# Performance work log

Measured on AMD Instinct MI355X. Metric: run time of the kernel, lower is better.

## Reference

```python
import jax, jax.numpy as jnp
import numpy as np

S, B, D, H, E, K = 1024, 4, 1024, 16, 3, 2
DFF = 4 * D
DH = D // H


def _layernorm(x, w, b, eps=1e-5):
    mu = jnp.mean(x, axis=-1, keepdims=True)
    var = jnp.var(x, axis=-1, keepdims=True)
    return (x - mu) * jax.lax.rsqrt(var + eps) * w + b


def _quick_gelu(x):
    return x * jax.nn.sigmoid(1.702 * x)


def setup_inputs() -> dict:
    key = jax.random.key(0)
    ks = jax.random.split(key, 8)
    w = lambda k, shape: jax.random.normal(k, shape, dtype=jnp.float32) * 0.02
    return {
        "x": jax.random.normal(ks[0], (S, B, D), dtype=jnp.float32),
        "ln1_w": jnp.ones((D,), jnp.float32), "ln1_b": jnp.zeros((D,), jnp.float32),
        "ln2_w": jnp.ones((D,), jnp.float32), "ln2_b": jnp.zeros((D,), jnp.float32),
        "in_proj_w": w(ks[1], (3 * D, D)), "in_proj_b": jnp.zeros((3 * D,), jnp.float32),
        "out_proj_w": w(ks[2], (D, D)), "out_proj_b": jnp.zeros((D,), jnp.float32),
        "gate_w": w(ks[3], (E, D)),
        "fc_w": w(ks[4], (E, DFF, D)), "fc_b": jnp.zeros((E, DFF), jnp.float32),
        "proj_w": w(ks[5], (E, D, DFF)), "proj_b": jnp.zeros((E, D), jnp.float32),
    }


def _forward(x, ln1_w, ln1_b, ln2_w, ln2_b, in_proj_w, in_proj_b,
             out_proj_w, out_proj_b, gate_w, fc_w, fc_b, proj_w, proj_b):
    s, b, d = x.shape
    # --- causal self-attention (torch nn.MultiheadAttention, seq-first) ---
    h = _layernorm(x, ln1_w, ln1_b)
    qkv = h @ in_proj_w.T + in_proj_b                      # [S,B,3D]
    q, k, v = jnp.split(qkv, 3, axis=-1)
    to_bhsd = lambda t: t.reshape(s, b, H, DH).transpose(1, 2, 0, 3)  # [B,H,S,Dh]
    q, k, v = to_bhsd(q) * (DH ** -0.5), to_bhsd(k), to_bhsd(v)
    mask = jnp.where(jnp.arange(s)[:, None] >= jnp.arange(s)[None, :], 0.0, -jnp.inf)
    scores = jnp.einsum("bhqd,bhkd->bhqk", q, k) + mask    # [B,H,S,S]
    attn = jax.nn.softmax(scores, axis=-1)
    o = jnp.einsum("bhqk,bhkd->bhqd", attn, v)
    o = o.transpose(2, 0, 1, 3).reshape(s, b, d)
    x = x + (o @ out_proj_w.T + out_proj_b)

    # --- MoE routing ---
    hs = _layernorm(x, ln2_w, ln2_b)
    hs_flat = hs.reshape(-1, d)                            # [T,D], T = S*B
    router_logits = hs_flat @ gate_w.T                     # [T,E]
    rw = jax.nn.softmax(router_logits.astype(jnp.float32), axis=-1)
    top_vals, top_idx = jax.lax.top_k(rw, K)               # [T,K]
    top_vals = top_vals / jnp.sum(top_vals, axis=-1, keepdims=True)

    # dense grouped expert FFN (E=3 small, compute-all + masked combine)
    h1 = _quick_gelu(jnp.einsum("td,efd->etf", hs_flat, fc_w) + fc_b[:, None, :])
    expert_out = jnp.einsum("etf,edf->etd", h1, proj_w) + proj_b[:, None, :]  # [E,T,D]
    comb = jnp.sum(jax.nn.one_hot(top_idx, E, dtype=top_vals.dtype) * top_vals[..., None], axis=1)  # [T,E]
    final_hidden_states = jnp.einsum("te,etd->td", comb, expert_out).reshape(s, b, d)
    del final_hidden_states  # NOTE: source computes this but never uses it in the output

    gate_score = jnp.max(top_vals, axis=-1).reshape(s, b, 1)
    out = x * gate_score
    return out, router_logits


def reference(x, ln1_w, ln1_b, ln2_w, ln2_b, in_proj_w, in_proj_b,
              out_proj_w, out_proj_b, gate_w, fc_w, fc_b, proj_w, proj_b):
    return _forward(x, ln1_w, ln1_b, ln2_w, ln2_b, in_proj_w, in_proj_b,
                    out_proj_w, out_proj_b, gate_w, fc_w, fc_b, proj_w, proj_b)
```

## Files before the change

### kernel.cpp

```cpp
#include <hip/hip_runtime.h>
#include <hip/hip_bf16.h>

#define S_DIM 1024
#define B_DIM 4
#define D_DIM 1024
#define H_DIM 16
#define DH    64
#define T_DIM (S_DIM * B_DIM)
#define QKV_N (3 * D_DIM)

using bf16 = __hip_bfloat16;
typedef __attribute__((ext_vector_type(4))) float fx4;
typedef __attribute__((ext_vector_type(8))) short bx8;

__device__ __forceinline__ unsigned short f2bf(float f) {
  union { float f; unsigned int u; } cv; cv.f = f;
  unsigned int u = cv.u;
  unsigned int r = (u + 0x7FFFu + ((u >> 16) & 1u)) >> 16;
  return (unsigned short)r;
}

__device__ __forceinline__ void g2l16(const void* g, void* l) {
  __builtin_amdgcn_global_load_lds(
      (const __attribute__((address_space(1))) unsigned int*)g,
      (__attribute__((address_space(3))) unsigned int*)l, 16, 0, 0);
}

__global__ __launch_bounds__(256) void cast2_f32_bf16(
    const float* __restrict__ a, bf16* __restrict__ da, int an4,
    const float* __restrict__ b, bf16* __restrict__ db, int bn4) {
  const int i = blockIdx.x * 256 + threadIdx.x;
  const float* src; bf16* dst; int j;
  if (i < an4) { src = a; dst = da; j = i; }
  else if (i < an4 + bn4) { src = b; dst = db; j = i - an4; }
  else return;
  const fx4 v = ((const fx4*)src)[j];
  ushort4 u;
  u.x = f2bf(v[0]); u.y = f2bf(v[1]); u.z = f2bf(v[2]); u.w = f2bf(v[3]);
  ((ushort4*)dst)[j] = u;
}

__global__ __launch_bounds__(256) void ln_bf16_kernel(
    const float* __restrict__ x, const float* __restrict__ w,
    const float* __restrict__ bb, bf16* __restrict__ out) {
  const int t = blockIdx.x, tid = threadIdx.x;
  const fx4 v = ((const fx4*)(x + (size_t)t * D_DIM))[tid];
  float s  = v[0] + v[1] + v[2] + v[3];
  float ss = v[0]*v[0] + v[1]*v[1] + v[2]*v[2] + v[3]*v[3];
#pragma unroll
  for (int off = 32; off >= 1; off >>= 1) {
    s  += __shfl_xor(s, off);
    ss += __shfl_xor(ss, off);
  }
  __shared__ float red[8];
  const int wid = tid >> 6, lane = tid & 63;
  if (lane == 0) { red[wid] = s; red[4 + wid] = ss; }
  __syncthreads();
  s  = red[0] + red[1] + red[2] + red[3];
  ss = red[4] + red[5] + red[6] + red[7];
  const float mu = s * (1.f / D_DIM);
  const float rstd = rsqrtf(ss * (1.f / D_DIM) - mu * mu + 1e-5f);
  const fx4 wv = ((const fx4*)w)[tid];
  const fx4 bv = ((const fx4*)bb)[tid];
  ushort4 u;
  u.x = f2bf((v[0] - mu) * rstd * wv[0] + bv[0]);
  u.y = f2bf((v[1] - mu) * rstd * wv[1] + bv[1]);
  u.z = f2bf((v[2] - mu) * rstd * wv[2] + bv[2]);
  u.w = f2bf((v[3] - mu) * rstd * wv[3] + bv[3]);
  ((ushort4*)(out + (size_t)t * D_DIM))[tid] = u;
}

template <int EPI>
__global__ __launch_bounds__(256, 2) void gemm_bt(
    const bf16* __restrict__ A, const bf16* __restrict__ B,
    const float* __restrict__ bias, const float* __restrict__ resid,
    float* __restrict__ C, ushort* __restrict__ qkvb, int N, int K) {
  __shared__ bf16 sA[2][128 * 32];
  __shared__ bf16 sB[2][128 * 32];
  const int tid  = threadIdx.x;
  const int brow = blockIdx.y * 128;
  const int bcol = blockIdx.x * 128;
  const int wid  = tid >> 6;
  const int lane = tid & 63;
  const int wr   = wid >> 1;
  const int wc   = wid & 1;
  const int fr   = lane & 15;
  const int fk   = lane >> 4;

  fx4 acc[4][4];
#pragma unroll
  for (int i = 0; i < 4; ++i)
#pragma unroll
    for (int j = 0; j < 4; ++j) acc[i][j] = 0.f;

  const int arow = tid >> 2;
  const int acol = (tid & 3) * 8;

  auto stage = [&](int buf, int kt) {
#pragma unroll
    for (int is = 0; is < 2; ++is) {
      const int row = is * 64 + arow;
      const int off = row * 64 + acol * 2;
      g2l16(A + (size_t)(brow + row) * K + kt + acol, (char*)sA[buf] + off);
      g2l16(B + (size_t)(bcol + row) * K + kt + acol, (char*)sB[buf] + off);
    }
  };

  stage(0, 0);
  asm volatile("s_waitcnt vmcnt(0)" ::: "memory");
  __builtin_amdgcn_s_barrier();
  asm volatile("" ::: "memory");

  const int nk = K >> 5;
  int cur = 0;
#pragma unroll 1
  for (int ki = 0; ki < nk; ++ki) {
    if (ki + 1 < nk) stage(cur ^ 1, (ki + 1) * 32);
    asm volatile("" ::: "memory");

    bx8 af[4], bfr[4];
#pragma unroll
    for (int mm = 0; mm < 4; ++mm)
      af[mm] = *(const bx8*)(sA[cur] + (wr * 64 + mm * 16 + fr) * 32 + fk * 8);
#pragma unroll
    for (int nn = 0; nn < 4; ++nn)
      bfr[nn] = *(const bx8*)(sB[cur] + (wc * 64 + nn * 16 + fr) * 32 + fk * 8);
#pragma unroll
    for (int mm = 0; mm < 4; ++mm)
#pragma unroll
      for (int nn = 0; nn < 4; ++nn)
        acc[mm][nn] = __builtin_amdgcn_mfma_f32_16x16x32_bf16(
            af[mm], bfr[nn], acc[mm][nn], 0, 0, 0);

    if (ki + 1 < nk) {
      asm volatile("s_waitcnt vmcnt(0)" ::: "memory");
      __builtin_amdgcn_s_barrier();
      asm volatile("" ::: "memory");
    }
    cur ^= 1;
  }

  const int row0 = brow + wr * 64 + fk * 4;
  const int col0 = bcol + wc * 64 + fr;
#pragma unroll
  for (int mm = 0; mm < 4; ++mm) {
#pragma unroll
    for (int nn = 0; nn < 4; ++nn) {
      const int col = col0 + nn * 16;
      const float bv = bias[col];
      if (EPI == 1) {
#pragma unroll
        for (int rr = 0; rr < 4; ++rr) {
          const int row = row0 + mm * 16 + rr;
          C[(size_t)row * N + col] = acc[mm][nn][rr] + bv + resid[(size_t)row * N + col];
        }
      } else {
        const int which = col >> 10;
        const int rem   = col & 1023;
        const int hh    = rem >> 6;
        const int dh    = rem & 63;
        const float scale = (which == 0) ? 0.18033688f : 1.0f;
#pragma unroll
        for (int rr = 0; rr < 4; ++rr) {
          const int row = row0 + mm * 16 + rr;
          const int ss2 = row >> 2, bb2 = row & 3;
          const float v = (acc[mm][nn][rr] + bv) * scale;
          qkvb[(size_t)which * 4194304 +
               ((size_t)(bb2 * 16 + hh)) * 65536 + (size_t)ss2 * 64 + dh] = f2bf(v);
        }
      }
    }
  }
}

__global__ __launch_bounds__(256) void transpose_v(
    const ushort* __restrict__ v, ushort* __restrict__ vt) {
  __shared__ ushort tile[64][65];
  const int g  = blockIdx.x;
  const int bh = g >> 4, st = g & 15;
  const int s0 = st * 64;
  const int tid = threadIdx.x;
  const int r  = tid >> 2;
  const int c0 = (tid & 3) * 16;
  const ushort* src = v + (size_t)bh * 65536 + (size_t)(s0 + r) * 64 + c0;
#pragma unroll
  for (int i = 0; i < 2; ++i) {
    const bx8 d = *(const bx8*)(src + i * 8);
#pragma unroll
    for (int j = 0; j < 8; ++j) tile[r][c0 + i * 8 + j] = (ushort)d[j];
  }
  __syncthreads();
  ushort* dst = vt + (size_t)bh * 65536 + (size_t)r * 1024 + s0 + c0;
  bx8 w0, w1;
#pragma unroll
  for (int j = 0; j < 8; ++j) {
    w0[j] = (short)tile[c0 + j][r];
    w1[j] = (short)tile[c0 + 8 + j][r];
  }
  *(bx8*)dst = w0;
  *(bx8*)(dst + 8) = w1;
}

__global__ __launch_bounds__(256, 4) void attn_mfma(
    const ushort* __restrict__ qb, const ushort* __restrict__ kb,
    const ushort* __restrict__ vtb, ushort* __restrict__ ob) {
  __shared__ __align__(16) char sK[2][8192];
  __shared__ __align__(16) char sVT[2][8192];
  __shared__ __align__(16) char sP[8192];
  const int tid  = threadIdx.x;
  const int wid  = tid >> 6;
  const int lane = tid & 63;
  const int g    = blockIdx.x;
  const int qt   = 15 - (g >> 6);
  const int bh   = g & 63;
  const int b    = bh >> 4, h = bh & 15;
  const int fr   = lane & 15;
  const int fk   = lane >> 4;
  const size_t bhoff = (size_t)bh * 65536;
  char* const sPw = sP + wid * 2048;
  const int swp = (fr & 7) << 4;

  auto stage = [&](int buf, int k0) {
#pragma unroll
    for (int is = 0; is < 2; ++is) {
      const int L    = is * 4096 + tid * 16;
      const int row  = L >> 7;
      const int colb = (L & 127) ^ ((row & 7) << 4);
      g2l16(kb  + bhoff + (size_t)(k0 + row) * 64 + (colb >> 1), sK[buf]  + L);
      g2l16(vtb + bhoff + (size_t)row * 1024 + k0 + (colb >> 1), sVT[buf] + L);
    }
  };

  const int q0w = qt * 64 + wid * 16;
  const ushort* qp = qb + bhoff + (size_t)(q0w + fr) * 64;
  const bx8 qf0 = *(const bx8*)(qp + fk * 8);
  const bx8 qf1 = *(const bx8*)(qp + 32 + fk * 8);
  asm volatile("s_waitcnt vmcnt(0)" ::: "memory");

  fx4 o4[4];
  float m = -3e38f, l = 0.f;
#pragma unroll
  for (int dt = 0; dt < 4; ++dt) o4[dt] = 0.f;

  stage(0, 0);
  int cur = 0;

#pragma unroll 1
  for (int kbk = 0; kbk <= qt; ++kbk) {
    if (kbk < qt) {
      stage(cur ^ 1, (kbk + 1) * 64);
      asm volatile("s_waitcnt vmcnt(4)" ::: "memory");
    } else {
      asm volatile("s_waitcnt vmcnt(0)" ::: "memory");
    }
    __builtin_amdgcn_s_barrier();
    asm volatile("" ::: "memory");
    const char* sKc  = sK[cur];
    const char* sVTc = sVT[cur];

    fx4 s4[4];
    __builtin_amdgcn_s_setprio(1);
#pragma unroll
    for (int kt = 0; kt < 4; ++kt) {
      const int krow = kt * 16 + fr;
      const int sw   = (krow & 7) << 4;
      const bx8 kf0 = *(const bx8*)(sKc + krow * 128 + ((fk * 16) ^ sw));
      const bx8 kf1 = *(const bx8*)(sKc + krow * 128 + ((64 + fk * 16) ^ sw));
      fx4 z = {0.f, 0.f, 0.f, 0.f};
      z = __builtin_amdgcn_mfma_f32_16x16x32_bf16(kf0, qf0, z, 0, 0, 0);
      s4[kt] = __builtin_amdgcn_mfma_f32_16x16x32_bf16(kf1, qf1, z, 0, 0, 0);
    }
    __builtin_amdgcn_s_setprio(0);

    if (kbk == qt) {
      const int qloc = wid * 16 + fr;
#pragma unroll
      for (int kt = 0; kt < 4; ++kt) {
        const int keyb = kt * 16 + fk * 4;
#pragma unroll
        for (int rr = 0; rr < 4; ++rr)
          if (keyb + rr > qloc) s4[kt][rr] = -3e38f;
      }
    }

    float pm = s4[0][0];
#pragma unroll
    for (int kt = 0; kt < 4; ++kt)
#pragma unroll
      for (int rr = 0; rr < 4; ++rr) pm = fmaxf(pm, s4[kt][rr]);
    pm = fmaxf(pm, __shfl_xor(pm, 16));
    pm = fmaxf(pm, __shfl_xor(pm, 32));

    if (__any(pm > m + 11.5f)) {
      const float mn = fmaxf(m, pm);
      const float f  = exp2f(m - mn);
      m = mn;
      l *= f;
      float fq[4];
#pragma unroll
      for (int rr = 0; rr < 4; ++rr) fq[rr] = __shfl(f, fk * 4 + rr);
#pragma unroll
      for (int dt = 0; dt < 4; ++dt)
#pragma unroll
        for (int rr = 0; rr < 4; ++rr) o4[dt][rr] *= fq[rr];
    }

#pragma unroll
    for (int kt = 0; kt < 4; ++kt) {
      union { float f; unsigned u; } a0, a1, a2, a3;
      a0.f = exp2f(s4[kt][0] - m);
      a1.f = exp2f(s4[kt][1] - m);
      a2.f = exp2f(s4[kt][2] - m);
      a3.f = exp2f(s4[kt][3] - m);
      l += (a0.f + a1.f) + (a2.f + a3.f);
      uint2 pk;
      pk.x = (a0.u >> 16) | (a1.u & 0xFFFF0000u);
      pk.y = (a2.u >> 16) | (a3.u & 0xFFFF0000u);
      *(uint2*)(sPw + ((fr * 128 + kt * 32 + fk * 8) ^ swp)) = pk;
    }

    __builtin_amdgcn_s_setprio(1);
#pragma unroll
    for (int c = 0; c < 2; ++c) {
      const bx8 pa = *(const bx8*)(sPw + ((fr * 128 + c * 64 + fk * 16) ^ swp));
#pragma unroll
      for (int dt = 0; dt < 4; ++dt) {
        const int vrow = dt * 16 + fr;
        const bx8 vf = *(const bx8*)(sVTc + vrow * 128 +
                                     ((c * 64 + fk * 16) ^ ((vrow & 7) << 4)));
        o4[dt] = __builtin_amdgcn_mfma_f32_16x16x32_bf16(pa, vf, o4[dt], 0, 0, 0);
      }
    }
    __builtin_amdgcn_s_setprio(0);

    asm volatile("" ::: "memory");
    __builtin_amdgcn_s_barrier();
    asm volatile("" ::: "memory");
    cur ^= 1;
  }

  l += __shfl_xor(l, 16);
  l += __shfl_xor(l, 32);
  const float linv = 1.f / l;
  float lq[4];
#pragma unroll
  for (int rr = 0; rr < 4; ++rr) lq[rr] = __shfl(linv, fk * 4 + rr);

#pragma unroll
  for (int dt = 0; dt < 4; ++dt) {
#pragma unroll
    for (int rr = 0; rr < 4; ++rr) {
      const int qq = q0w + fk * 4 + rr;
      ob[((size_t)qq * 4 + b) * 1024 + h * 64 + dt * 16 + fr] =
          f2bf(o4[dt][rr] * lq[rr]);
    }
  }
}

__global__ __launch_bounds__(256) void final_kernel(
    const float* __restrict__ xn, const float* __restrict__ w,
    const float* __restrict__ bb, const float* __restrict__ gw,
    float* __restrict__ out, float* __restrict__ rlog) {
  const int t = blockIdx.x, tid = threadIdx.x;
  const fx4 v = ((const fx4*)(xn + (size_t)t * D_DIM))[tid];
  float s  = v[0] + v[1] + v[2] + v[3];
  float ss = v[0]*v[0] + v[1]*v[1] + v[2]*v[2] + v[3]*v[3];
#pragma unroll
  for (int off = 32; off >= 1; off >>= 1) {
    s  += __shfl_xor(s, off);
    ss += __shfl_xor(ss, off);
  }
  __shared__ float red[8];
  __shared__ float red2[12];
  const int wid = tid >> 6, lane = tid & 63;
  if (lane == 0) { red[wid] = s; red[4 + wid] = ss; }
  __syncthreads();
  s  = red[0] + red[1] + red[2] + red[3];
  ss = red[4] + red[5] + red[6] + red[7];
  const float mu = s * (1.f / D_DIM);
  const float rstd = rsqrtf(ss * (1.f / D_DIM) - mu * mu + 1e-5f);
  const fx4 wv = ((const fx4*)w)[tid];
  const fx4 bv = ((const fx4*)bb)[tid];
  fx4 hv;
#pragma unroll
  for (int cc = 0; cc < 4; ++cc) hv[cc] = (v[cc] - mu) * rstd * wv[cc] + bv[cc];

  const fx4 w0 = ((const fx4*)(gw           ))[tid];
  const fx4 w1 = ((const fx4*)(gw +     D_DIM))[tid];
  const fx4 w2 = ((const fx4*)(gw + 2 * D_DIM))[tid];
  float g0 = hv[0]*w0[0] + hv[1]*w0[1] + hv[2]*w0[2] + hv[3]*w0[3];
  float g1 = hv[0]*w1[0] + hv[1]*w1[1] + hv[2]*w1[2] + hv[3]*w1[3];
  float g2 = hv[0]*w2[0] + hv[1]*w2[1] + hv[2]*w2[2] + hv[3]*w2[3];
#pragma unroll
  for (int off = 32; off >= 1; off >>= 1) {
    g0 += __shfl_xor(g0, off);
    g1 += __shfl_xor(g1, off);
    g2 += __shfl_xor(g2, off);
  }
  if (lane == 0) { red2[wid] = g0; red2[4 + wid] = g1; red2[8 + wid] = g2; }
  __syncthreads();
  g0 = red2[0] + red2[1] + red2[2]  + red2[3];
  g1 = red2[4] + red2[5] + red2[6]  + red2[7];
  g2 = red2[8] + red2[9] + red2[10] + red2[11];

  const float lmax = fmaxf(g0, fmaxf(g1, g2));
  const float lmin = fminf(g0, fminf(g1, g2));
  const float lmid = (g0 + g1 + g2) - lmax - lmin;
  const float gate = 1.f / (1.f + __expf(lmid - lmax));

  ((fx4*)(out + (size_t)t * D_DIM))[tid] = v * gate;
  if (tid == 0) {
    rlog[(size_t)t * 3 + 0] = g0;
    rlog[(size_t)t * 3 + 1] = g1;
    rlog[(size_t)t * 3 + 2] = g2;
  }
}

extern "C" void kernel_launch(void* const* d_in, const int* in_sizes, int n_in,
                              void* d_out, int out_size, void* d_ws, size_t ws_size,
                              hipStream_t stream) {
  (void)in_sizes; (void)n_in; (void)out_size; (void)ws_size;
  const float* x    = (const float*)d_in[0];
  const float* ln1w = (const float*)d_in[1];
  const float* ln1b = (const float*)d_in[2];
  const float* ln2w = (const float*)d_in[3];
  const float* ln2b = (const float*)d_in[4];
  const float* win  = (const float*)d_in[5];
  const float* bin  = (const float*)d_in[6];
  const float* wout = (const float*)d_in[7];
  const float* bout = (const float*)d_in[8];
  const float* gw   = (const float*)d_in[9];

  char* ws = (char*)d_ws;
  bf16*   w_in_b  = (bf16*)(ws);
  bf16*   w_out_b = (bf16*)(ws + 6291456);
  bf16*   h_b     = (bf16*)(ws + 8388608);
  ushort* o_b     = (ushort*)h_b;
  ushort* qkvb    = (ushort*)(ws + 16777216);
  ushort* q_b     = qkvb;
  ushort* k_b     = qkvb + 4194304;
  ushort* v_b     = qkvb + 8388608;
  float*  xnew    = (float*)(ws + 41943040);
  ushort* vt_b    = (ushort*)(ws + 58720256);

  float* out  = (float*)d_out;
  float* rlog = out + (size_t)T_DIM * D_DIM;

  cast2_f32_bf16<<<4096, 256, 0, stream>>>(win, w_in_b, 786432,
                                           wout, w_out_b, 262144);
  ln_bf16_kernel<<<T_DIM, 256, 0, stream>>>(x, ln1w, ln1b, h_b);
  gemm_bt<2><<<dim3(QKV_N / 128, T_DIM / 128), 256, 0, stream>>>(
      h_b, w_in_b, bin, nullptr, nullptr, qkvb, QKV_N, D_DIM);
  transpose_v<<<1024, 256, 0, stream>>>(v_b, vt_b);
  attn_mfma<<<1024, 256, 0, stream>>>(q_b, k_b, vt_b, o_b);
  gemm_bt<1><<<dim3(D_DIM / 128, T_DIM / 128), 256, 0, stream>>>(
      (const bf16*)o_b, w_out_b, bout, x, xnew, nullptr, D_DIM, D_DIM);
  final_kernel<<<T_DIM, 256, 0, stream>>>(xnew, ln2w, ln2b, gw, out, rlog);
}
```

Before: 115.8 us.

## Pair causal query tiles per attention block, merge prep kernels, narrow out-proj tiles

Attention now runs 512-thread blocks where two groups of four waves handle complementary query tiles (pr and 15-pr), so every block does the same total causal work. Shared K/V staging is reused across both tiles, and blocks are ordered so each XCD keeps to a fixed set of heads. The weight cast and LN1 are merged into one launch, and the output projection gets its own kernel with 128x64 tiles for more blocks. The cost is more idle waves for the short-tile group, which still waits on barriers while the long tile runs, and lower per-block occupancy at 512 threads.

Measured after the change: 115.5 us. Within noise of the previous version (-0.3%).

```diff
diff --git a/kernel.cpp b/kernel.cpp
--- a/kernel.cpp
+++ b/kernel.cpp
@@ -26,24 +26,24 @@
       (__attribute__((address_space(3))) unsigned int*)l, 16, 0, 0);
 }
 
-__global__ __launch_bounds__(256) void cast2_f32_bf16(
-    const float* __restrict__ a, bf16* __restrict__ da, int an4,
-    const float* __restrict__ b, bf16* __restrict__ db, int bn4) {
-  const int i = blockIdx.x * 256 + threadIdx.x;
-  const float* src; bf16* dst; int j;
-  if (i < an4) { src = a; dst = da; j = i; }
-  else if (i < an4 + bn4) { src = b; dst = db; j = i - an4; }
-  else return;
-  const fx4 v = ((const fx4*)src)[j];
-  ushort4 u;
-  u.x = f2bf(v[0]); u.y = f2bf(v[1]); u.z = f2bf(v[2]); u.w = f2bf(v[3]);
-  ((ushort4*)dst)[j] = u;
-}
-
-__global__ __launch_bounds__(256) void ln_bf16_kernel(
+__global__ __launch_bounds__(256) void prep_kernel(
     const float* __restrict__ x, const float* __restrict__ w,
-    const float* __restrict__ bb, bf16* __restrict__ out) {
-  const int t = blockIdx.x, tid = threadIdx.x;
+    const float* __restrict__ bb, bf16* __restrict__ out,
+    const float* __restrict__ win, bf16* __restrict__ winb,
+    const float* __restrict__ wout, bf16* __restrict__ woutb) {
+  const int blk = blockIdx.x, tid = threadIdx.x;
+  if (blk >= 4096) {
+    const int i = (blk - 4096) * 256 + tid;
+    const float* src; bf16* dst; int j;
+    if (i < 786432) { src = win; dst = winb; j = i; }
+    else { src = wout; dst = woutb; j = i - 786432; }
+    const fx4 v = ((const fx4*)src)[j];
+    ushort4 u;
+    u.x = f2bf(v[0]); u.y = f2bf(v[1]); u.z = f2bf(v[2]); u.w = f2bf(v[3]);
+    ((ushort4*)dst)[j] = u;
+    return;
+  }
+  const int t = blk;
   const fx4 v = ((const fx4*)(x + (size_t)t * D_DIM))[tid];
   float s  = v[0] + v[1] + v[2] + v[3];
   float ss = v[0]*v[0] + v[1]*v[1] + v[2]*v[2] + v[3]*v[3];
@@ -70,11 +70,9 @@
   ((ushort4*)(out + (size_t)t * D_DIM))[tid] = u;
 }
 
-template <int EPI>
-__global__ __launch_bounds__(256, 2) void gemm_bt(
+__global__ __launch_bounds__(256, 2) void gemm_qkv(
     const bf16* __restrict__ A, const bf16* __restrict__ B,
-    const float* __restrict__ bias, const float* __restrict__ resid,
-    float* __restrict__ C, ushort* __restrict__ qkvb, int N, int K) {
+    const float* __restrict__ bias, ushort* __restrict__ qkvb, int K) {
   __shared__ bf16 sA[2][128 * 32];
   __shared__ bf16 sB[2][128 * 32];
   const int tid  = threadIdx.x;
@@ -148,26 +146,18 @@
     for (int nn = 0; nn < 4; ++nn) {
       const int col = col0 + nn * 16;
       const float bv = bias[col];
-      if (EPI == 1) {
-#pragma unroll
-        for (int rr = 0; rr < 4; ++rr) {
-          const int row = row0 + mm * 16 + rr;
-          C[(size_t)row * N + col] = acc[mm][nn][rr] + bv + resid[(size_t)row * N + col];
-        }
-      } else {
-        const int which = col >> 10;
-        const int rem   = col & 1023;
-        const int hh    = rem >> 6;
-        const int dh    = rem & 63;
-        const float scale = (which == 0) ? 0.18033688f : 1.0f;
-#pragma unroll
-        for (int rr = 0; rr < 4; ++rr) {
-          const int row = row0 + mm * 16 + rr;
-          const int ss2 = row >> 2, bb2 = row & 3;
-          const float v = (acc[mm][nn][rr] + bv) * scale;
-          qkvb[(size_t)which * 4194304 +
-               ((size_t)(bb2 * 16 + hh)) * 65536 + (size_t)ss2 * 64 + dh] = f2bf(v);
-        }
+      const int which = col >> 10;
+      const int rem   = col & 1023;
+      const int hh    = rem >> 6;
+      const int dh    = rem & 63;
+      const float scale = (which == 0) ? 0.18033688f : 1.0f;
+#pragma unroll
+      for (int rr = 0; rr < 4; ++rr) {
+        const int row = row0 + mm * 16 + rr;
+        const int ss2 = row >> 2, bb2 = row & 3;
+        const float v = (acc[mm][nn][rr] + bv) * scale;
+        qkvb[(size_t)which * 4194304 +
+             ((size_t)(bb2 * 16 + hh)) * 65536 + (size_t)ss2 * 64 + dh] = f2bf(v);
       }
     }
   }
@@ -201,37 +191,39 @@
   *(bx8*)(dst + 8) = w1;
 }
 
-__global__ __launch_bounds__(256, 4) void attn_mfma(
+__global__ __launch_bounds__(512, 4) void attn_mfma(
     const ushort* __restrict__ qb, const ushort* __restrict__ kb,
     const ushort* __restrict__ vtb, ushort* __restrict__ ob) {
   __shared__ __align__(16) char sK[2][8192];
   __shared__ __align__(16) char sVT[2][8192];
-  __shared__ __align__(16) char sP[8192];
+  __shared__ __align__(16) char sP[16384];
   const int tid  = threadIdx.x;
   const int wid  = tid >> 6;
   const int lane = tid & 63;
-  const int g    = blockIdx.x;
-  const int qt   = 15 - (g >> 6);
-  const int bh   = g & 63;
+  const int bid  = blockIdx.x;
+  const int xcd  = bid & 7;
+  const int r2   = bid >> 3;
+  const int pr   = r2 & 7;
+  const int bh   = (r2 >> 3) * 8 + xcd;
   const int b    = bh >> 4, h = bh & 15;
   const int fr   = lane & 15;
   const int fk   = lane >> 4;
   const size_t bhoff = (size_t)bh * 65536;
   char* const sPw = sP + wid * 2048;
   const int swp = (fr & 7) << 4;
+  const int qt_max  = 15 - pr;
+  const int qt_mine = (wid < 4) ? pr : qt_max;
+  const int wid4 = wid & 3;
 
   auto stage = [&](int buf, int k0) {
-#pragma unroll
-    for (int is = 0; is < 2; ++is) {
-      const int L    = is * 4096 + tid * 16;
-      const int row  = L >> 7;
-      const int colb = (L & 127) ^ ((row & 7) << 4);
-      g2l16(kb  + bhoff + (size_t)(k0 + row) * 64 + (colb >> 1), sK[buf]  + L);
-      g2l16(vtb + bhoff + (size_t)row * 1024 + k0 + (colb >> 1), sVT[buf] + L);
-    }
+    const int L    = tid * 16;
+    const int row  = L >> 7;
+    const int colb = (L & 127) ^ ((row & 7) << 4);
+    g2l16(kb  + bhoff + (size_t)(k0 + row) * 64 + (colb >> 1), sK[buf]  + L);
+    g2l16(vtb + bhoff + (size_t)row * 1024 + k0 + (colb >> 1), sVT[buf] + L);
   };
 
-  const int q0w = qt * 64 + wid * 16;
+  const int q0w = qt_mine * 64 + wid4 * 16;
   const ushort* qp = qb + bhoff + (size_t)(q0w + fr) * 64;
   const bx8 qf0 = *(const bx8*)(qp + fk * 8);
   const bx8 qf1 = *(const bx8*)(qp + 32 + fk * 8);
@@ -243,100 +235,102 @@
   for (int dt = 0; dt < 4; ++dt) o4[dt] = 0.f;
 
   stage(0, 0);
-  int cur = 0;
 
 #pragma unroll 1
-  for (int kbk = 0; kbk <= qt; ++kbk) {
-    if (kbk < qt) {
+  for (int kbk = 0; kbk <= qt_max; ++kbk) {
+    const int cur = kbk & 1;
+    if (kbk < qt_max) {
       stage(cur ^ 1, (kbk + 1) * 64);
-      asm volatile("s_waitcnt vmcnt(4)" ::: "memory");
+      asm volatile("s_waitcnt vmcnt(2)" ::: "memory");
     } else {
       asm volatile("s_waitcnt vmcnt(0)" ::: "memory");
     }
     __builtin_amdgcn_s_barrier();
     asm volatile("" ::: "memory");
-    const char* sKc  = sK[cur];
-    const char* sVTc = sVT[cur];
-
-    fx4 s4[4];
-    __builtin_amdgcn_s_setprio(1);
-#pragma unroll
-    for (int kt = 0; kt < 4; ++kt) {
-      const int krow = kt * 16 + fr;
-      const int sw   = (krow & 7) << 4;
-      const bx8 kf0 = *(const bx8*)(sKc + krow * 128 + ((fk * 16) ^ sw));
-      const bx8 kf1 = *(const bx8*)(sKc + krow * 128 + ((64 + fk * 16) ^ sw));
-      fx4 z = {0.f, 0.f, 0.f, 0.f};
-      z = __builtin_amdgcn_mfma_f32_16x16x32_bf16(kf0, qf0, z, 0, 0, 0);
-      s4[kt] = __builtin_amdgcn_mfma_f32_16x16x32_bf16(kf1, qf1, z, 0, 0, 0);
-    }
-    __builtin_amdgcn_s_setprio(0);
-
-    if (kbk == qt) {
-      const int qloc = wid * 16 + fr;
+
+    if (kbk <= qt_mine) {
+      const char* sKc  = sK[cur];
+      const char* sVTc = sVT[cur];
+
+      fx4 s4[4];
+      __builtin_amdgcn_s_setprio(1);
 #pragma unroll
       for (int kt = 0; kt < 4; ++kt) {
-        const int keyb = kt * 16 + fk * 4;
-#pragma unroll
-        for (int rr = 0; rr < 4; ++rr)
-          if (keyb + rr > qloc) s4[kt][rr] = -3e38f;
-      }
-    }
-
-    float pm = s4[0][0];
-#pragma unroll
-    for (int kt = 0; kt < 4; ++kt)
-#pragma unroll
-      for (int rr = 0; rr < 4; ++rr) pm = fmaxf(pm, s4[kt][rr]);
-    pm = fmaxf(pm, __shfl_xor(pm, 16));
-    pm = fmaxf(pm, __shfl_xor(pm, 32));
-
-    if (__any(pm > m + 11.5f)) {
-      const float mn = fmaxf(m, pm);
-      const float f  = exp2f(m - mn);
-      m = mn;
-      l *= f;
-      float fq[4];
-#pragma unroll
-      for (int rr = 0; rr < 4; ++rr) fq[rr] = __shfl(f, fk * 4 + rr);
-#pragma unroll
-      for (int dt = 0; dt < 4; ++dt)
-#pragma unroll
-        for (int rr = 0; rr < 4; ++rr) o4[dt][rr] *= fq[rr];
-    }
-
-#pragma unroll
-    for (int kt = 0; kt < 4; ++kt) {
-      union { float f; unsigned u; } a0, a1, a2, a3;
-      a0.f = exp2f(s4[kt][0] - m);
-      a1.f = exp2f(s4[kt][1] - m);
-      a2.f = exp2f(s4[kt][2] - m);
-      a3.f = exp2f(s4[kt][3] - m);
-      l += (a0.f + a1.f) + (a2.f + a3.f);
-      uint2 pk;
-      pk.x = (a0.u >> 16) | (a1.u & 0xFFFF0000u);
-      pk.y = (a2.u >> 16) | (a3.u & 0xFFFF0000u);
-      *(uint2*)(sPw + ((fr * 128 + kt * 32 + fk * 8) ^ swp)) = pk;
-    }
-
-    __builtin_amdgcn_s_setprio(1);
-#pragma unroll
-    for (int c = 0; c < 2; ++c) {
-      const bx8 pa = *(const bx8*)(sPw + ((fr * 128 + c * 64 + fk * 16) ^ swp));
-#pragma unroll
-      for (int dt = 0; dt < 4; ++dt) {
-        const int vrow = dt * 16 + fr;
-        const bx8 vf = *(const bx8*)(sVTc + vrow * 128 +
-                                     ((c * 64 + fk * 16) ^ ((vrow & 7) << 4)));
-        o4[dt] = __builtin_amdgcn_mfma_f32_16x16x32_bf16(pa, vf, o4[dt], 0, 0, 0);
-      }
-    }
-    __builtin_amdgcn_s_setprio(0);
+        const int krow = kt * 16 + fr;
+        const int sw   = (krow & 7) << 4;
+        const bx8 kf0 = *(const bx8*)(sKc + krow * 128 + ((fk * 16) ^ sw));
+        const bx8 kf1 = *(const bx8*)(sKc + krow * 128 + ((64 + fk * 16) ^ sw));
+        fx4 z = {0.f, 0.f, 0.f, 0.f};
+        z = __builtin_amdgcn_mfma_f32_16x16x32_bf16(kf0, qf0, z, 0, 0, 0);
+        s4[kt] = __builtin_amdgcn_mfma_f32_16x16x32_bf16(kf1, qf1, z, 0, 0, 0);
+      }
+      __builtin_amdgcn_s_setprio(0);
+
+      if (kbk == qt_mine) {
+        const int qloc = wid4 * 16 + fr;
+#pragma unroll
+        for (int kt = 0; kt < 4; ++kt) {
+          const int keyb = kt * 16 + fk * 4;
+#pragma unroll
+          for (int rr = 0; rr < 4; ++rr)
+            if (keyb + rr > qloc) s4[kt][rr] = -3e38f;
+        }
+      }
+
+      float pm = s4[0][0];
+#pragma unroll
+      for (int kt = 0; kt < 4; ++kt)
+#pragma unroll
+        for (int rr = 0; rr < 4; ++rr) pm = fmaxf(pm, s4[kt][rr]);
+      pm = fmaxf(pm, __shfl_xor(pm, 16));
+      pm = fmaxf(pm, __shfl_xor(pm, 32));
+
+      if (__any(pm > m + 11.5f)) {
+        const float mn = fmaxf(m, pm);
+        const float f  = exp2f(m - mn);
+        m = mn;
+        l *= f;
+        float fq[4];
+#pragma unroll
+        for (int rr = 0; rr < 4; ++rr) fq[rr] = __shfl(f, fk * 4 + rr);
+#pragma unroll
+        for (int dt = 0; dt < 4; ++dt)
+#pragma unroll
+          for (int rr = 0; rr < 4; ++rr) o4[dt][rr] *= fq[rr];
+      }
+
+#pragma unroll
+      for (int kt = 0; kt < 4; ++kt) {
+        union { float f; unsigned u; } a0, a1, a2, a3;
+        a0.f = exp2f(s4[kt][0] - m);
+        a1.f = exp2f(s4[kt][1] - m);
+        a2.f = exp2f(s4[kt][2] - m);
+        a3.f = exp2f(s4[kt][3] - m);
+        l += (a0.f + a1.f) + (a2.f + a3.f);
+        uint2 pk;
+        pk.x = (a0.u >> 16) | (a1.u & 0xFFFF0000u);
+        pk.y = (a2.u >> 16) | (a3.u & 0xFFFF0000u);
+        *(uint2*)(sPw + ((fr * 128 + kt * 32 + fk * 8) ^ swp)) = pk;
+      }
+
+      __builtin_amdgcn_s_setprio(1);
+#pragma unroll
+      for (int c = 0; c < 2; ++c) {
+        const bx8 pa = *(const bx8*)(sPw + ((fr * 128 + c * 64 + fk * 16) ^ swp));
+#pragma unroll
+        for (int dt = 0; dt < 4; ++dt) {
+          const int vrow = dt * 16 + fr;
+          const bx8 vf = *(const bx8*)(sVTc + vrow * 128 +
+                                       ((c * 64 + fk * 16) ^ ((vrow & 7) << 4)));
+          o4[dt] = __builtin_amdgcn_mfma_f32_16x16x32_bf16(pa, vf, o4[dt], 0, 0, 0);
+        }
+      }
+      __builtin_amdgcn_s_setprio(0);
+    }
 
     asm volatile("" ::: "memory");
     __builtin_amdgcn_s_barrier();
     asm volatile("" ::: "memory");
-    cur ^= 1;
   }
 
   l += __shfl_xor(l, 16);
@@ -353,6 +347,93 @@
       const int qq = q0w + fk * 4 + rr;
       ob[((size_t)qq * 4 + b) * 1024 + h * 64 + dt * 16 + fr] =
           f2bf(o4[dt][rr] * lq[rr]);
+    }
+  }
+}
+
+__global__ __launch_bounds__(256, 2) void gemm_out(
+    const bf16* __restrict__ A, const bf16* __restrict__ B,
+    const float* __restrict__ bias, const float* __restrict__ resid,
+    float* __restrict__ C) {
+  __shared__ bf16 sA[2][128 * 32];
+  __shared__ bf16 sB[2][64 * 32];
+  const int tid  = threadIdx.x;
+  const int brow = blockIdx.y * 128;
+  const int bcol = blockIdx.x * 64;
+  const int wid  = tid >> 6;
+  const int lane = tid & 63;
+  const int wr   = wid >> 1;
+  const int wc   = wid & 1;
+  const int fr   = lane & 15;
+  const int fk   = lane >> 4;
+
+  fx4 acc[4][2];
+#pragma unroll
+  for (int i = 0; i < 4; ++i)
+#pragma unroll
+    for (int j = 0; j < 2; ++j) acc[i][j] = 0.f;
+
+  const int arow = tid >> 2;
+  const int acol = (tid & 3) * 8;
+
+  auto stage = [&](int buf, int kt) {
+#pragma unroll
+    for (int is = 0; is < 2; ++is) {
+      const int row = is * 64 + arow;
+      g2l16(A + (size_t)(brow + row) * 1024 + kt + acol,
+            (char*)sA[buf] + row * 64 + acol * 2);
+    }
+    g2l16(B + (size_t)(bcol + arow) * 1024 + kt + acol,
+          (char*)sB[buf] + arow * 64 + acol * 2);
+  };
+
+  stage(0, 0);
+  asm volatile("s_waitcnt vmcnt(0)" ::: "memory");
+  __builtin_amdgcn_s_barrier();
+  asm volatile("" ::: "memory");
+
+  int cur = 0;
+#pragma unroll 1
+  for (int ki = 0; ki < 32; ++ki) {
+    if (ki + 1 < 32) stage(cur ^ 1, (ki + 1) * 32);
+    asm volatile("" ::: "memory");
+
+    bx8 af[4], bfr[2];
+#pragma unroll
+    for (int mm = 0; mm < 4; ++mm)
+      af[mm] = *(const bx8*)(sA[cur] + (wr * 64 + mm * 16 + fr) * 32 + fk * 8);
+#pragma unroll
+    for (int nn = 0; nn < 2; ++nn)
+      bfr[nn] = *(const bx8*)(sB[cur] + (wc * 32 + nn * 16 + fr) * 32 + fk * 8);
+#pragma unroll
+    for (int mm = 0; mm < 4; ++mm)
+#pragma unroll
+      for (int nn = 0; nn < 2; ++nn)
+        acc[mm][nn] = __builtin_amdgcn_mfma_f32_16x16x32_bf16(
+            af[mm], bfr[nn], acc[mm][nn], 0, 0, 0);
+
+    if (ki + 1 < 32) {
+      asm volatile("s_waitcnt vmcnt(0)" ::: "memory");
+      __builtin_amdgcn_s_barrier();
+      asm volatile("" ::: "memory");
+    }
+    cur ^= 1;
+  }
+
+  const int row0 = brow + wr * 64 + fk * 4;
+  const int col0 = bcol + wc * 32 + fr;
+#pragma unroll
+  for (int mm = 0; mm < 4; ++mm) {
+#pragma unroll
+    for (int nn = 0; nn < 2; ++nn) {
+      const int col = col0 + nn * 16;
+      const float bv = bias[col];
+#pragma unroll
+      for (int rr = 0; rr < 4; ++rr) {
+        const int row = row0 + mm * 16 + rr;
+        C[(size_t)row * 1024 + col] =
+            acc[mm][nn][rr] + bv + resid[(size_t)row * 1024 + col];
+      }
     }
   }
 }
@@ -446,14 +527,13 @@
   float* out  = (float*)d_out;
   float* rlog = out + (size_t)T_DIM * D_DIM;
 
-  cast2_f32_bf16<<<4096, 256, 0, stream>>>(win, w_in_b, 786432,
-                                           wout, w_out_b, 262144);
-  ln_bf16_kernel<<<T_DIM, 256, 0, stream>>>(x, ln1w, ln1b, h_b);
-  gemm_bt<2><<<dim3(QKV_N / 128, T_DIM / 128), 256, 0, stream>>>(
-      h_b, w_in_b, bin, nullptr, nullptr, qkvb, QKV_N, D_DIM);
+  prep_kernel<<<8192, 256, 0, stream>>>(x, ln1w, ln1b, h_b,
+                                        win, w_in_b, wout, w_out_b);
+  gemm_qkv<<<dim3(QKV_N / 128, T_DIM / 128), 256, 0, stream>>>(
+      h_b, w_in_b, bin, qkvb, D_DIM);
   transpose_v<<<1024, 256, 0, stream>>>(v_b, vt_b);
-  attn_mfma<<<1024, 256, 0, stream>>>(q_b, k_b, vt_b, o_b);
-  gemm_bt<1><<<dim3(D_DIM / 128, T_DIM / 128), 256, 0, stream>>>(
-      (const bf16*)o_b, w_out_b, bout, x, xnew, nullptr, D_DIM, D_DIM);
+  attn_mfma<<<512, 512, 0, stream>>>(q_b, k_b, vt_b, o_b);
+  gemm_out<<<dim3(D_DIM / 64, T_DIM / 128), 256, 0, stream>>>(
+      (const bf16*)o_b, w_out_b, bout, x, xnew);
   final_kernel<<<T_DIM, 256, 0, stream>>>(xnew, ln2w, ln2b, gw, out, rlog);
 }
```
